# Kernel tuning notes

Measured on AMD Instinct MI355X. Metric: run time of the kernel, lower is better.

The kernel has to match this reference:

```python
import jax, jax.numpy as jnp
import numpy as np

NEG_SLOPE = 0.2
EPS = 1e-16

N_NODES = 100000
N_EDGES = 1600000
IN_CH = 128
HEADS = 4
OUT_CH = 32


def setup_inputs() -> dict:
    key = jax.random.key(0)
    k1, k2, k3, k4, k5 = jax.random.split(key, 5)
    x = jax.random.normal(k1, (N_NODES, IN_CH), dtype=jnp.float32)
    edge_index = jax.random.randint(k2, (2, N_EDGES), 0, N_NODES, dtype=jnp.int64)
    glorot = (6.0 / (IN_CH + HEADS * OUT_CH)) ** 0.5
    W_l = jax.random.uniform(k3, (IN_CH, HEADS * OUT_CH), jnp.float32, -glorot, glorot)
    W_r = jax.random.uniform(k4, (IN_CH, HEADS * OUT_CH), jnp.float32, -glorot, glorot)
    ga = (6.0 / (OUT_CH + 1)) ** 0.5
    att = jax.random.uniform(k5, (HEADS, OUT_CH), jnp.float32, -ga, ga)
    bias = jnp.zeros((HEADS * OUT_CH,), dtype=jnp.float32)
    return {"x": x, "edge_index": edge_index, "W_l": W_l, "W_r": W_r, "att": att, "bias": bias}


def reference(x, edge_index, W_l, W_r, att, bias):
    # GATv2Conv forward (PyG semantics, concat=True, add_self_loops=False)
    N = x.shape[0]
    H, C = att.shape
    src, dst = edge_index[0], edge_index[1]

    x_l = (x @ W_l).reshape(N, H, C)  # source transform
    x_r = (x @ W_r).reshape(N, H, C)  # target transform

    # per-edge attention logits: e_ij = att . leaky_relu(x_l[j] + x_r[i])
    h = x_l[src] + x_r[dst]                      # [E, H, C]
    e = jnp.einsum('ehc,hc->eh', jax.nn.leaky_relu(h, NEG_SLOPE), att)  # [E, H]

    # segment softmax over edges grouped by destination node
    m = jax.ops.segment_max(e, dst, num_segments=N)      # [N, H]
    e_exp = jnp.exp(e - m[dst])                          # [E, H]
    denom = jax.ops.segment_sum(e_exp, dst, num_segments=N)  # [N, H]
    alpha = e_exp / (denom[dst] + EPS)                   # [E, H]

    # attention-weighted message aggregation
    msg = x_l[src] * alpha[:, :, None]                   # [E, H, C]
    out = jax.ops.segment_sum(msg, dst, num_segments=N)  # [N, H, C]
    return out.reshape(N, H * C) + bias
```

## Files before the change

### kernel.cpp

```cpp
#include <hip/hip_runtime.h>
#include <hip/hip_bf16.h>
#include <cstdint>
#include <cstddef>


#define NEG_SLOPE 0.2f
#define EPS_F 1e-16f
#define NRANGE 8
#define NCHUNK 32
#define SORT_B 1024
#define MAX_RSZ 12512

typedef __attribute__((ext_vector_type(8))) short bf16x8;
typedef __attribute__((ext_vector_type(4))) float f32x4;

static __device__ __forceinline__ unsigned f2bf(float f) {
    unsigned u = __float_as_uint(f);
    return (u + 0x7fffu + ((u >> 16) & 1u)) >> 16;
}
static __device__ __forceinline__ float bf2f(unsigned h) {
    return __uint_as_float(h << 16);
}
static __device__ __forceinline__ float bflo(unsigned u) {
    return __uint_as_float(u << 16);
}
static __device__ __forceinline__ float bfhi(unsigned u) {
    return __uint_as_float(u & 0xffff0000u);
}

__global__ __launch_bounds__(SORT_B) void histW_k(const int* __restrict__ dst, int E, int N,
                                                  int rsz, int chunk_e,
                                                  unsigned short* __restrict__ g,
                                                  const float* __restrict__ Wl,
                                                  const float* __restrict__ Wr,
                                                  unsigned short* __restrict__ Wtl,
                                                  unsigned short* __restrict__ Wtr) {
    if (blockIdx.x == NRANGE * NCHUNK) {
        for (int mat = 0; mat < 2; ++mat) {
            const float* W = mat ? Wr : Wl;
            unsigned short* Wt = mat ? Wtr : Wtl;
            for (int i = 0; i < 16; ++i) {
                int idx = (int)threadIdx.x + i * SORT_B;
                int k = idx >> 7, n = idx & 127;
                Wt[n * 128 + k] = (unsigned short)f2bf(W[idx]);
            }
        }
        return;
    }
    __shared__ unsigned lcnt[MAX_RSZ];
    const int r = blockIdx.x & (NRANGE - 1);
    const int c = blockIdx.x >> 3;
    const unsigned r_lo = (unsigned)(r * rsz);
    const int e0 = c * chunk_e;
    const int e1 = min(e0 + chunk_e, E);

    for (int i = threadIdx.x; i < rsz; i += SORT_B) lcnt[i] = 0u;
    __syncthreads();

    int e_vec_end = e0;
    if ((((uintptr_t)(dst + e0)) & 15) == 0) {
        const int nq = (e1 - e0) >> 2;
        const int4* dq = (const int4*)(dst + e0);
        for (int q = (int)threadIdx.x; q < nq; q += SORT_B) {
            int4 d4 = dq[q];
            unsigned dd;
            dd = (unsigned)d4.x - r_lo; if (dd < (unsigned)rsz) atomicAdd(&lcnt[dd], 1u);
            dd = (unsigned)d4.y - r_lo; if (dd < (unsigned)rsz) atomicAdd(&lcnt[dd], 1u);
            dd = (unsigned)d4.z - r_lo; if (dd < (unsigned)rsz) atomicAdd(&lcnt[dd], 1u);
            dd = (unsigned)d4.w - r_lo; if (dd < (unsigned)rsz) atomicAdd(&lcnt[dd], 1u);
        }
        e_vec_end = e0 + (nq << 2);
    }
    for (int e = e_vec_end + (int)threadIdx.x; e < e1; e += SORT_B) {
        unsigned dd = (unsigned)dst[e] - r_lo;
        if (dd < (unsigned)rsz) atomicAdd(&lcnt[dd], 1u);
    }
    __syncthreads();
    unsigned short* gc = g + (size_t)c * N + r_lo;
    int lim = min(rsz, N - (int)r_lo);
    for (int i = threadIdx.x; i < lim; i += SORT_B) gc[i] = (unsigned short)lcnt[i];
}

#define LROW 136
__global__ __launch_bounds__(256) void mfma_gemm_k(const float* __restrict__ A,
                                                   const unsigned short* __restrict__ Wtl,
                                                   const unsigned short* __restrict__ Wtr,
                                                   unsigned short* __restrict__ xl,
                                                   unsigned short* __restrict__ xr,
                                                   int nrows) {
    __shared__ unsigned short As[64 * LROW];
    __shared__ unsigned short Ws[128 * LROW];
    const int tid = threadIdx.x;
    const int wave = tid >> 6, lane = tid & 63;
    const int quad = lane >> 4, m16 = lane & 15;
    const int row0 = blockIdx.x * 64;

#pragma unroll
    for (int i = 0; i < 8; ++i) {
        int idx = tid + i * 256;
        int r = idx >> 5, c4 = idx & 31;
        int gr = row0 + r;
        gr = gr < nrows ? gr : nrows - 1;
        float4 v = *(const float4*)(A + (size_t)gr * 128 + c4 * 4);
        ushort4 b;
        b.x = (unsigned short)f2bf(v.x);
        b.y = (unsigned short)f2bf(v.y);
        b.z = (unsigned short)f2bf(v.z);
        b.w = (unsigned short)f2bf(v.w);
        *(ushort4*)(&As[r * LROW + c4 * 4]) = b;
    }
#pragma unroll
    for (int i = 0; i < 8; ++i) {
        int idx = tid + i * 256;
        int n = idx >> 4, kq = idx & 15;
        *(uint4*)(&Ws[n * LROW + kq * 8]) = *(const uint4*)(Wtl + n * 128 + kq * 8);
    }
    __syncthreads();

    bf16x8 af[4];
#pragma unroll
    for (int ks = 0; ks < 4; ++ks)
        af[ks] = *(const bf16x8*)(&As[(wave * 16 + m16) * LROW + ks * 32 + quad * 8]);

    f32x4 acc[8];
#pragma unroll
    for (int ct = 0; ct < 8; ++ct) acc[ct] = (f32x4){0.f, 0.f, 0.f, 0.f};
#pragma unroll
    for (int ct = 0; ct < 8; ++ct)
#pragma unroll
        for (int ks = 0; ks < 4; ++ks) {
            bf16x8 bf = *(const bf16x8*)(&Ws[(ct * 16 + m16) * LROW + ks * 32 + quad * 8]);
            acc[ct] = __builtin_amdgcn_mfma_f32_16x16x32_bf16(af[ks], bf, acc[ct], 0, 0, 0);
        }
#pragma unroll
    for (int ct = 0; ct < 8; ++ct)
#pragma unroll
        for (int r = 0; r < 4; ++r) {
            int grow = row0 + wave * 16 + quad * 4 + r;
            if (grow < nrows) xl[(size_t)grow * 128 + ct * 16 + m16] = (unsigned short)f2bf(acc[ct][r]);
        }

    __syncthreads();
#pragma unroll
    for (int i = 0; i < 8; ++i) {
        int idx = tid + i * 256;
        int n = idx >> 4, kq = idx & 15;
        *(uint4*)(&Ws[n * LROW + kq * 8]) = *(const uint4*)(Wtr + n * 128 + kq * 8);
    }
    __syncthreads();

#pragma unroll
    for (int ct = 0; ct < 8; ++ct) acc[ct] = (f32x4){0.f, 0.f, 0.f, 0.f};
#pragma unroll
    for (int ct = 0; ct < 8; ++ct)
#pragma unroll
        for (int ks = 0; ks < 4; ++ks) {
            bf16x8 bf = *(const bf16x8*)(&Ws[(ct * 16 + m16) * LROW + ks * 32 + quad * 8]);
            acc[ct] = __builtin_amdgcn_mfma_f32_16x16x32_bf16(af[ks], bf, acc[ct], 0, 0, 0);
        }
#pragma unroll
    for (int ct = 0; ct < 8; ++ct)
#pragma unroll
        for (int r = 0; r < 4; ++r) {
            int grow = row0 + wave * 16 + quad * 4 + r;
            if (grow < nrows) xr[(size_t)grow * 128 + ct * 16 + m16] = (unsigned short)f2bf(acc[ct][r]);
        }
}

#define SCAN_B 256
__global__ __launch_bounds__(SCAN_B) void scanA_k(const unsigned short* __restrict__ g, int n,
                                                  int* __restrict__ row_start,
                                                  int* __restrict__ bsum) {
    const int tid = threadIdx.x, lane = tid & 63, wid = tid >> 6;
    const int d = blockIdx.x * SCAN_B + tid;
    int v = 0;
    if (d < n) {
        unsigned s = 0;
#pragma unroll
        for (int c = 0; c < NCHUNK; ++c) s += g[(size_t)c * n + d];
        v = (int)s;
    }
    int inc = v;
#pragma unroll
    for (int dd = 1; dd < 64; dd <<= 1) {
        int t = __shfl_up(inc, dd);
        if (lane >= dd) inc += t;
    }
    __shared__ int wsum[SCAN_B / 64];
    if (lane == 63) wsum[wid] = inc;
    __syncthreads();
    int add = 0;
    for (int w = 0; w < wid; ++w) add += wsum[w];
    inc += add;
    if (d < n) row_start[d] = inc - v;
    if (tid == SCAN_B - 1) bsum[blockIdx.x] = inc;
}

__global__ __launch_bounds__(512) void scanB_k(int* __restrict__ bsum, int nb) {
    const int tid = threadIdx.x, lane = tid & 63, wid = tid >> 6;
    int v = (tid < nb) ? bsum[tid] : 0;
    int inc = v;
#pragma unroll
    for (int d = 1; d < 64; d <<= 1) {
        int t = __shfl_up(inc, d);
        if (lane >= d) inc += t;
    }
    __shared__ int wsum[8];
    if (lane == 63) wsum[wid] = inc;
    __syncthreads();
    int add = 0;
    for (int w = 0; w < wid; ++w) add += wsum[w];
    inc += add;
    if (tid < nb) bsum[tid] = inc - v;
}

__global__ __launch_bounds__(SCAN_B) void scanCb_k(int* __restrict__ row_start,
                                                   const int* __restrict__ bsum,
                                                   const unsigned short* __restrict__ g,
                                                   int N, int E,
                                                   int* __restrict__ src_sorted,
                                                   unsigned* __restrict__ base) {
    const int d = blockIdx.x * SCAN_B + threadIdx.x;
    if (blockIdx.x == 0 && threadIdx.x == 0) row_start[N] = E;
    if (blockIdx.x == 0 && threadIdx.x < 16) src_sorted[E + threadIdx.x] = 0;
    if (d >= N) return;
    unsigned run = (unsigned)(row_start[d] + bsum[blockIdx.x]);
    row_start[d] = (int)run;
#pragma unroll
    for (int c = 0; c < NCHUNK; ++c) {
        base[(size_t)c * N + d] = run;
        run += g[(size_t)c * N + d];
    }
}

__global__ __launch_bounds__(SORT_B) void scat_k(const int* __restrict__ src,
                                                 const int* __restrict__ dst, int E, int N,
                                                 int rsz, int chunk_e,
                                                 const unsigned* __restrict__ base,
                                                 int* __restrict__ src_sorted) {
    __shared__ unsigned lcur[MAX_RSZ];
    const int r = blockIdx.x & (NRANGE - 1);
    const int c = blockIdx.x >> 3;
    const unsigned r_lo = (unsigned)(r * rsz);
    const int e0 = c * chunk_e;
    const int e1 = min(e0 + chunk_e, E);

    const unsigned* bc = base + (size_t)c * N + r_lo;
    int lim = min(rsz, N - (int)r_lo);
    for (int i = threadIdx.x; i < lim; i += SORT_B) lcur[i] = bc[i];
    __syncthreads();

    int e_vec_end = e0;
    if (((((uintptr_t)(dst + e0)) | ((uintptr_t)(src + e0))) & 15) == 0) {
        const int nq = (e1 - e0) >> 2;
        const int4* dq = (const int4*)(dst + e0);
        const int4* sq = (const int4*)(src + e0);
        for (int q = (int)threadIdx.x; q < nq; q += SORT_B) {
            int4 d4 = dq[q];
            int4 s4 = sq[q];
            unsigned dd;
            dd = (unsigned)d4.x - r_lo;
            if (dd < (unsigned)rsz) { unsigned pos = atomicAdd(&lcur[dd], 1u); src_sorted[pos] = s4.x << 8; }
            dd = (unsigned)d4.y - r_lo;
            if (dd < (unsigned)rsz) { unsigned pos = atomicAdd(&lcur[dd], 1u); src_sorted[pos] = s4.y << 8; }
            dd = (unsigned)d4.z - r_lo;
            if (dd < (unsigned)rsz) { unsigned pos = atomicAdd(&lcur[dd], 1u); src_sorted[pos] = s4.z << 8; }
            dd = (unsigned)d4.w - r_lo;
            if (dd < (unsigned)rsz) { unsigned pos = atomicAdd(&lcur[dd], 1u); src_sorted[pos] = s4.w << 8; }
        }
        e_vec_end = e0 + (nq << 2);
    }
    for (int e = e_vec_end + (int)threadIdx.x; e < e1; e += SORT_B) {
        unsigned dd = (unsigned)dst[e] - r_lo;
        if (dd < (unsigned)rsz) {
            unsigned pos = atomicAdd(&lcur[dd], 1u);
            src_sorted[pos] = src[e] << 8;
        }
    }
}

__global__ __launch_bounds__(256) void agg_k(const unsigned* __restrict__ xlb,
                                             const unsigned* __restrict__ xrb,
                                             const float* __restrict__ att,
                                             const float* __restrict__ bias,
                                             const int* __restrict__ row_start,
                                             const int* __restrict__ src_sorted,
                                             int n, float* __restrict__ out) {
    const int wave = threadIdx.x >> 6;
    const int lane = threadIdx.x & 63;
    const int i = blockIdx.x * 4 + wave;
    if (i >= n) return;

    const int sub = lane & 15;
    const int eg  = lane >> 4;
    const int cb  = sub * 16;
    const char* xb = (const char*)xlb;

    uint4 xrv = *(const uint4*)(xrb + (size_t)i * 64 + sub * 4);
    const float xr0 = bflo(xrv.x), xr1 = bfhi(xrv.x);
    const float xr2 = bflo(xrv.y), xr3 = bfhi(xrv.y);
    const float xr4 = bflo(xrv.z), xr5 = bfhi(xrv.z);
    const float xr6 = bflo(xrv.w), xr7 = bfhi(xrv.w);

    const float L2E = 1.44269504088896f;
    float4 atA = *(const float4*)(att + sub * 8);
    float4 atB = *(const float4*)(att + sub * 8 + 4);
    atA.x *= L2E; atA.y *= L2E; atA.z *= L2E; atA.w *= L2E;
    atB.x *= L2E; atB.y *= L2E; atB.z *= L2E; atB.w *= L2E;

    const int k0 = row_start[i];
    const int k1 = row_start[i + 1];

    float l = 0.f;
    float A0 = 0.f, A1 = 0.f, A2 = 0.f, A3 = 0.f;
    float A4 = 0.f, A5 = 0.f, A6 = 0.f, A7 = 0.f;

#define PROC_GRP(V, OFF)                                                       \
    {                                                                          \
        float x0 = bflo(V.x), x1 = bfhi(V.x);                                  \
        float x2 = bflo(V.y), x3 = bfhi(V.y);                                  \
        float x4 = bflo(V.z), x5 = bfhi(V.z);                                  \
        float x6 = bflo(V.w), x7 = bfhi(V.w);                                  \
        float h0 = x0 + xr0, h1 = x1 + xr1, h2 = x2 + xr2, h3 = x3 + xr3;      \
        float h4 = x4 + xr4, h5 = x5 + xr5, h6 = x6 + xr6, h7 = x7 + xr7;      \
        float t, p;                                                            \
        t = fmaxf(h0, NEG_SLOPE * h0); p = atA.x * t;                          \
        t = fmaxf(h1, NEG_SLOPE * h1); p = fmaf(atA.y, t, p);                  \
        t = fmaxf(h2, NEG_SLOPE * h2); p = fmaf(atA.z, t, p);                  \
        t = fmaxf(h3, NEG_SLOPE * h3); p = fmaf(atA.w, t, p);                  \
        t = fmaxf(h4, NEG_SLOPE * h4); p = fmaf(atB.x, t, p);                  \
        t = fmaxf(h5, NEG_SLOPE * h5); p = fmaf(atB.y, t, p);                  \
        t = fmaxf(h6, NEG_SLOPE * h6); p = fmaf(atB.z, t, p);                  \
        t = fmaxf(h7, NEG_SLOPE * h7); p = fmaf(atB.w, t, p);                  \
        p += __shfl_xor(p, 1);                                                 \
        p += __shfl_xor(p, 2);                                                 \
        float w;                                                               \
        asm("v_exp_f32 %0, %1" : "=v"(w) : "v"(p));                            \
        w = (k + (OFF) + eg < k1) ? w : 0.f;                                   \
        l += w;                                                                \
        A0 = fmaf(w, x0, A0); A1 = fmaf(w, x1, A1);                            \
        A2 = fmaf(w, x2, A2); A3 = fmaf(w, x3, A3);                            \
        A4 = fmaf(w, x4, A4); A5 = fmaf(w, x5, A5);                            \
        A6 = fmaf(w, x6, A6); A7 = fmaf(w, x7, A7);                            \
    }

    for (int k = k0; k < k1; k += 16) {
        int sA = src_sorted[k + eg];
        int sB = src_sorted[k + 4 + eg];
        int sC = src_sorted[k + 8 + eg];
        int sD = src_sorted[k + 12 + eg];
        uint4 vA = *(const uint4*)(xb + (unsigned)sA + cb);
        uint4 vB = *(const uint4*)(xb + (unsigned)sB + cb);
        uint4 vC = *(const uint4*)(xb + (unsigned)sC + cb);
        uint4 vD = *(const uint4*)(xb + (unsigned)sD + cb);

        PROC_GRP(vA, 0)
        PROC_GRP(vB, 4)
        PROC_GRP(vC, 8)
        PROC_GRP(vD, 12)
    }
#undef PROC_GRP

    l  += __shfl_xor(l, 16);  l  += __shfl_xor(l, 32);
    A0 += __shfl_xor(A0, 16); A0 += __shfl_xor(A0, 32);
    A1 += __shfl_xor(A1, 16); A1 += __shfl_xor(A1, 32);
    A2 += __shfl_xor(A2, 16); A2 += __shfl_xor(A2, 32);
    A3 += __shfl_xor(A3, 16); A3 += __shfl_xor(A3, 32);
    A4 += __shfl_xor(A4, 16); A4 += __shfl_xor(A4, 32);
    A5 += __shfl_xor(A5, 16); A5 += __shfl_xor(A5, 32);
    A6 += __shfl_xor(A6, 16); A6 += __shfl_xor(A6, 32);
    A7 += __shfl_xor(A7, 16); A7 += __shfl_xor(A7, 32);

    if (eg == 0) {
        float inv = 1.f / (l + EPS_F);
        float4 b0 = *(const float4*)(bias + sub * 8);
        float4 b1 = *(const float4*)(bias + sub * 8 + 4);
        float4 o0 = {fmaf(A0, inv, b0.x), fmaf(A1, inv, b0.y),
                     fmaf(A2, inv, b0.z), fmaf(A3, inv, b0.w)};
        float4 o1 = {fmaf(A4, inv, b1.x), fmaf(A5, inv, b1.y),
                     fmaf(A6, inv, b1.z), fmaf(A7, inv, b1.w)};
        *(float4*)(out + (size_t)i * 128 + sub * 8)     = o0;
        *(float4*)(out + (size_t)i * 128 + sub * 8 + 4) = o1;
    }
}

extern "C" void kernel_launch(void* const* d_in, const int* in_sizes, int n_in,
                              void* d_out, int out_size, void* d_ws, size_t ws_size,
                              hipStream_t stream) {
    const float* x    = (const float*)d_in[0];
    const int*   ei   = (const int*)d_in[1];
    const float* W_l  = (const float*)d_in[2];
    const float* W_r  = (const float*)d_in[3];
    const float* att  = (const float*)d_in[4];
    const float* bias = (const float*)d_in[5];
    float* out = (float*)d_out;

    const int N = in_sizes[0] / 128;
    const int E = in_sizes[1] / 2;
    const int* src = ei;
    const int* dst = ei + E;

    char* ws = (char*)d_ws;
    size_t off = 0;
    auto alloc = [&](size_t bytes) {
        void* p = ws + off;
        off += (bytes + 15) & ~(size_t)15;
        return p;
    };
    unsigned* xlb       = (unsigned*)alloc((size_t)N * 64 * 4);
    unsigned* xrb       = (unsigned*)alloc((size_t)N * 64 * 4);
    unsigned short* g   = (unsigned short*)alloc((size_t)NCHUNK * N * 2);
    unsigned* base      = (unsigned*)alloc((size_t)NCHUNK * N * 4);
    int* row_start      = (int*)alloc((size_t)(N + 1) * 4);
    const int nsb = (N + SCAN_B - 1) / SCAN_B;
    int* bsum           = (int*)alloc((size_t)nsb * 4);
    int* src_sorted     = (int*)alloc((size_t)(E + 16) * 4);
    unsigned short* Wtl = (unsigned short*)alloc((size_t)128 * 128 * 2);
    unsigned short* Wtr = (unsigned short*)alloc((size_t)128 * 128 * 2);
    (void)ws_size;

    const int rsz = (N + NRANGE - 1) / NRANGE;
    int chunk_e = (E + NCHUNK - 1) / NCHUNK;
    chunk_e = (chunk_e + 3) & ~3;

    histW_k<<<NRANGE * NCHUNK + 1, SORT_B, 0, stream>>>(dst, E, N, rsz, chunk_e, g,
                                                        W_l, W_r, Wtl, Wtr);

    const int gB = (N + 63) / 64;
    mfma_gemm_k<<<gB, 256, 0, stream>>>(x, Wtl, Wtr,
                                        (unsigned short*)xlb, (unsigned short*)xrb, N);

    scanA_k<<<nsb, SCAN_B, 0, stream>>>(g, N, row_start, bsum);
    scanB_k<<<1, 512, 0, stream>>>(bsum, nsb);
    scanCb_k<<<nsb, SCAN_B, 0, stream>>>(row_start, bsum, g, N, E, src_sorted, base);

    scat_k<<<NRANGE * NCHUNK, SORT_B, 0, stream>>>(src, dst, E, N, rsz, chunk_e,
                                                   base, src_sorted);

    agg_k<<<(N + 3) / 4, 256, 0, stream>>>(xlb, xrb, att, bias, row_start, src_sorted, N, out);
}
```

Baseline: 282.9 us.

## Use packed f32x2 math in aggregation and halve per-iteration edge unroll

Rewrites the per-edge attention and accumulation math in the aggregation kernel with two-wide float vectors, so the compiler can emit packed FP32 instructions (v_pk_add/mul/fma). It also cuts the loop step from 16 to 8 edges per iteration and clamps out-of-range source indices to 0 before the gather. Processing fewer padded edges per node should cut wasted gathers and math for low-degree nodes, at the cost of less memory-level parallelism per iteration. The clamp keeps tail loads in bounds.

```diff
diff --git a/kernel.cpp b/kernel.cpp
--- a/kernel.cpp
+++ b/kernel.cpp
@@ -13,6 +13,7 @@
 
 typedef __attribute__((ext_vector_type(8))) short bf16x8;
 typedef __attribute__((ext_vector_type(4))) float f32x4;
+typedef __attribute__((ext_vector_type(2))) float f32x2;
 
 static __device__ __forceinline__ unsigned f2bf(float f) {
     unsigned u = __float_as_uint(f);
@@ -297,69 +298,74 @@
     const char* xb = (const char*)xlb;
 
     uint4 xrv = *(const uint4*)(xrb + (size_t)i * 64 + sub * 4);
-    const float xr0 = bflo(xrv.x), xr1 = bfhi(xrv.x);
-    const float xr2 = bflo(xrv.y), xr3 = bfhi(xrv.y);
-    const float xr4 = bflo(xrv.z), xr5 = bfhi(xrv.z);
-    const float xr6 = bflo(xrv.w), xr7 = bfhi(xrv.w);
+    const f32x2 xr01 = {bflo(xrv.x), bfhi(xrv.x)};
+    const f32x2 xr23 = {bflo(xrv.y), bfhi(xrv.y)};
+    const f32x2 xr45 = {bflo(xrv.z), bfhi(xrv.z)};
+    const f32x2 xr67 = {bflo(xrv.w), bfhi(xrv.w)};
 
     const float L2E = 1.44269504088896f;
-    float4 atA = *(const float4*)(att + sub * 8);
-    float4 atB = *(const float4*)(att + sub * 8 + 4);
-    atA.x *= L2E; atA.y *= L2E; atA.z *= L2E; atA.w *= L2E;
-    atB.x *= L2E; atB.y *= L2E; atB.z *= L2E; atB.w *= L2E;
+    float4 a0 = *(const float4*)(att + sub * 8);
+    float4 a1 = *(const float4*)(att + sub * 8 + 4);
+    const f32x2 at01 = {a0.x * L2E, a0.y * L2E};
+    const f32x2 at23 = {a0.z * L2E, a0.w * L2E};
+    const f32x2 at45 = {a1.x * L2E, a1.y * L2E};
+    const f32x2 at67 = {a1.z * L2E, a1.w * L2E};
+    const f32x2 ns2 = {NEG_SLOPE, NEG_SLOPE};
 
     const int k0 = row_start[i];
     const int k1 = row_start[i + 1];
 
     float l = 0.f;
-    float A0 = 0.f, A1 = 0.f, A2 = 0.f, A3 = 0.f;
-    float A4 = 0.f, A5 = 0.f, A6 = 0.f, A7 = 0.f;
+    f32x2 Ac01 = {0.f, 0.f}, Ac23 = {0.f, 0.f};
+    f32x2 Ac45 = {0.f, 0.f}, Ac67 = {0.f, 0.f};
 
 #define PROC_GRP(V, OFF)                                                       \
     {                                                                          \
-        float x0 = bflo(V.x), x1 = bfhi(V.x);                                  \
-        float x2 = bflo(V.y), x3 = bfhi(V.y);                                  \
-        float x4 = bflo(V.z), x5 = bfhi(V.z);                                  \
-        float x6 = bflo(V.w), x7 = bfhi(V.w);                                  \
-        float h0 = x0 + xr0, h1 = x1 + xr1, h2 = x2 + xr2, h3 = x3 + xr3;      \
-        float h4 = x4 + xr4, h5 = x5 + xr5, h6 = x6 + xr6, h7 = x7 + xr7;      \
-        float t, p;                                                            \
-        t = fmaxf(h0, NEG_SLOPE * h0); p = atA.x * t;                          \
-        t = fmaxf(h1, NEG_SLOPE * h1); p = fmaf(atA.y, t, p);                  \
-        t = fmaxf(h2, NEG_SLOPE * h2); p = fmaf(atA.z, t, p);                  \
-        t = fmaxf(h3, NEG_SLOPE * h3); p = fmaf(atA.w, t, p);                  \
-        t = fmaxf(h4, NEG_SLOPE * h4); p = fmaf(atB.x, t, p);                  \
-        t = fmaxf(h5, NEG_SLOPE * h5); p = fmaf(atB.y, t, p);                  \
-        t = fmaxf(h6, NEG_SLOPE * h6); p = fmaf(atB.z, t, p);                  \
-        t = fmaxf(h7, NEG_SLOPE * h7); p = fmaf(atB.w, t, p);                  \
+        f32x2 x01 = {bflo(V.x), bfhi(V.x)};                                    \
+        f32x2 x23 = {bflo(V.y), bfhi(V.y)};                                    \
+        f32x2 x45 = {bflo(V.z), bfhi(V.z)};                                    \
+        f32x2 x67 = {bflo(V.w), bfhi(V.w)};                                    \
+        f32x2 h01 = x01 + xr01, h23 = x23 + xr23;                              \
+        f32x2 h45 = x45 + xr45, h67 = x67 + xr67;                              \
+        f32x2 m01 = h01 * ns2, m23 = h23 * ns2;                                \
+        f32x2 m45 = h45 * ns2, m67 = h67 * ns2;                                \
+        f32x2 t01 = {fmaxf(h01.x, m01.x), fmaxf(h01.y, m01.y)};                \
+        f32x2 t23 = {fmaxf(h23.x, m23.x), fmaxf(h23.y, m23.y)};                \
+        f32x2 t45 = {fmaxf(h45.x, m45.x), fmaxf(h45.y, m45.y)};                \
+        f32x2 t67 = {fmaxf(h67.x, m67.x), fmaxf(h67.y, m67.y)};                \
+        f32x2 pa = at01 * t01;                                                 \
+        pa = __builtin_elementwise_fma(at23, t23, pa);                         \
+        pa = __builtin_elementwise_fma(at45, t45, pa);                         \
+        pa = __builtin_elementwise_fma(at67, t67, pa);                         \
+        float p = pa.x + pa.y;                                                 \
         p += __shfl_xor(p, 1);                                                 \
         p += __shfl_xor(p, 2);                                                 \
         float w;                                                               \
         asm("v_exp_f32 %0, %1" : "=v"(w) : "v"(p));                            \
         w = (k + (OFF) + eg < k1) ? w : 0.f;                                   \
         l += w;                                                                \
-        A0 = fmaf(w, x0, A0); A1 = fmaf(w, x1, A1);                            \
-        A2 = fmaf(w, x2, A2); A3 = fmaf(w, x3, A3);                            \
-        A4 = fmaf(w, x4, A4); A5 = fmaf(w, x5, A5);                            \
-        A6 = fmaf(w, x6, A6); A7 = fmaf(w, x7, A7);                            \
-    }
-
-    for (int k = k0; k < k1; k += 16) {
+        f32x2 w2 = {w, w};                                                     \
+        Ac01 = __builtin_elementwise_fma(w2, x01, Ac01);                       \
+        Ac23 = __builtin_elementwise_fma(w2, x23, Ac23);                       \
+        Ac45 = __builtin_elementwise_fma(w2, x45, Ac45);                       \
+        Ac67 = __builtin_elementwise_fma(w2, x67, Ac67);                       \
+    }
+
+    for (int k = k0; k < k1; k += 8) {
         int sA = src_sorted[k + eg];
         int sB = src_sorted[k + 4 + eg];
-        int sC = src_sorted[k + 8 + eg];
-        int sD = src_sorted[k + 12 + eg];
+        sA = (k + eg < k1) ? sA : 0;
+        sB = (k + 4 + eg < k1) ? sB : 0;
         uint4 vA = *(const uint4*)(xb + (unsigned)sA + cb);
         uint4 vB = *(const uint4*)(xb + (unsigned)sB + cb);
-        uint4 vC = *(const uint4*)(xb + (unsigned)sC + cb);
-        uint4 vD = *(const uint4*)(xb + (unsigned)sD + cb);
 
         PROC_GRP(vA, 0)
         PROC_GRP(vB, 4)
-        PROC_GRP(vC, 8)
-        PROC_GRP(vD, 12)
     }
 #undef PROC_GRP
+
+    float A0 = Ac01.x, A1 = Ac01.y, A2 = Ac23.x, A3 = Ac23.y;
+    float A4 = Ac45.x, A5 = Ac45.y, A6 = Ac67.x, A7 = Ac67.y;
 
     l  += __shfl_xor(l, 16);  l  += __shfl_xor(l, 32);
     A0 += __shfl_xor(A0, 16); A0 += __shfl_xor(A0, 32);
```

Result: faster. 273.7 us (-3.3%).
